# Optimization experiments

Hardware: AMD Instinct MI355X
Metric: run time of the kernel (lower is better)

Reference implementation:

```python
import jax, jax.numpy as jnp
import numpy as np

DIM = 8          # per-head dim
ATT_EPS = 1e-15
BN_EPS = 1e-6


def setup_inputs() -> dict:
    key = jax.random.key(0)
    ks = jax.random.split(key, 6)
    B, C, H, W = 8, 256, 64, 64
    td = 256                      # heads * dim = 32 * 8
    return {
        'x':      jax.random.normal(ks[0], (B, C, H, W), jnp.float32),
        'w_qkv':  jax.random.normal(ks[1], (3 * td, C), jnp.float32) * 0.05,
        'w_dw':   jax.random.normal(ks[2], (3 * td, 1, 5, 5), jnp.float32) * 0.05,
        'w_pw':   jax.random.normal(ks[3], (96, 8, 8), jnp.float32) * 0.05,   # (groups, out/g, in/g)
        'w_proj': jax.random.normal(ks[4], (C, 2 * td), jnp.float32) * 0.05,
        'bn_gamma': jnp.ones((C,), jnp.float32),
        'bn_beta':  jnp.zeros((C,), jnp.float32),
        'bn_mean':  jnp.zeros((C,), jnp.float32),
        'bn_var':   jnp.ones((C,), jnp.float32),
    }


def _relu_linear_att(ms, H, W):
    # ms: [B, C, H, W] with C = heads * 3*DIM
    B = ms.shape[0]
    d = DIM
    qkv = ms.reshape(B, -1, 3 * d, H * W).transpose(0, 1, 3, 2)   # [B, h, N, 3d]
    q = jax.nn.relu(qkv[..., :d])
    k = jax.nn.relu(qkv[..., d:2 * d])
    v = qkv[..., 2 * d:]
    v = jnp.pad(v, ((0, 0), (0, 0), (0, 0), (0, 1)), constant_values=1.0)  # ones column
    kv = jnp.einsum('bhnd,bhne->bhde', k, v)                       # [B, h, d, d+1]
    out = jnp.einsum('bhnd,bhde->bhne', q, kv)                     # [B, h, N, d+1]
    out = out[..., :-1] / (out[..., -1:] + ATT_EPS)
    return out.transpose(0, 1, 3, 2).reshape(B, -1, H, W)          # [B, h*d, H, W]


def reference(x, w_qkv, w_dw, w_pw, w_proj, bn_gamma, bn_beta, bn_mean, bn_var):
    B, C, H, W = x.shape
    # 1x1 qkv projection
    qkv = jnp.einsum('oc,bchw->bohw', w_qkv, x)                    # [B, 768, H, W]
    # multiscale aggregation: 5x5 depthwise then grouped 1x1 (groups = 3*heads = 96)
    dw = jax.lax.conv_general_dilated(
        qkv, w_dw, window_strides=(1, 1), padding=[(2, 2), (2, 2)],
        dimension_numbers=('NCHW', 'OIHW', 'NCHW'),
        feature_group_count=qkv.shape[1])
    G, O, I = w_pw.shape
    agg = jnp.einsum('goi,bgihw->bgohw', w_pw,
                     dw.reshape(B, G, I, H, W)).reshape(B, G * O, H, W)
    ms = jnp.concatenate([qkv, agg], axis=1)                       # [B, 1536, H, W]
    att = _relu_linear_att(ms, H, W)                               # [B, 512, H, W]
    # proj: 1x1 conv + BatchNorm (eval mode) + identity activation
    p = jnp.einsum('oc,bchw->bohw', w_proj, att)                   # [B, 256, H, W]
    inv = bn_gamma / jnp.sqrt(bn_var + BN_EPS)
    p = p * inv[None, :, None, None] + (bn_beta - bn_mean * inv)[None, :, None, None]
    return x + p
```

## Files before the change

### kernel.cpp

```cpp
#include <hip/hip_runtime.h>
#include <hip/hip_bf16.h>


#define HW 4096
#define ATT_EPS 1e-15f
#define BN_EPS 1e-6f

typedef __attribute__((ext_vector_type(8))) short short8;
typedef __attribute__((ext_vector_type(4))) short short4v;
typedef __attribute__((ext_vector_type(4))) float f32x4;
typedef __attribute__((ext_vector_type(2))) float f32x2;
typedef __attribute__((ext_vector_type(8))) unsigned short u16x8;
typedef __attribute__((ext_vector_type(4))) unsigned short u16x4;

static __device__ inline short f2bf(float f) {
    union { float f; unsigned u; } v; v.f = f;
    unsigned r = v.u + 0x7fff + ((v.u >> 16) & 1);
    return (short)(r >> 16);
}
static __device__ inline float bf2f(unsigned short u) {
    union { unsigned u; float f; } v; v.u = (unsigned)u << 16; return v.f;
}

__global__ __launch_bounds__(256) void prep_w(const float* __restrict__ wproj,
                                              unsigned short* __restrict__ wbf) {
    const int i = (blockIdx.x * 256 + threadIdx.x) * 4;
    float4 v = *(const float4*)&wproj[i];
    u16x4 r = {(unsigned short)f2bf(v.x), (unsigned short)f2bf(v.y),
               (unsigned short)f2bf(v.z), (unsigned short)f2bf(v.w)};
    *(u16x4*)&wbf[i] = r;
}

__global__ __launch_bounds__(256) void qkv_gemm(const float* __restrict__ x,
                                                const float* __restrict__ w,
                                                unsigned short* __restrict__ qkv) {
    __shared__ short A_l[128 * 40];
    __shared__ short B_l[128 * 40];
    const int t  = threadIdx.x;
    const int b  = blockIdx.z;
    const int ob = blockIdx.y * 128;
    const int nb = blockIdx.x * 128;
    const float* xb = x + (size_t)b * 256 * HW;

    const int lane = t & 63, wave = t >> 6;
    const int wo = (wave >> 1) * 64, wn = (wave & 1) * 64;

    f32x4 acc[4][4];
#pragma unroll
    for (int s = 0; s < 4; s++)
#pragma unroll
        for (int u = 0; u < 4; u++) acc[s][u] = (f32x4){0.f, 0.f, 0.f, 0.f};

    const int col4 = (t & 7) * 4;
    const int r0   = t >> 3;
    for (int kb = 0; kb < 256; kb += 32) {
        __syncthreads();
#pragma unroll
        for (int i = 0; i < 4; i++) {
            const int r = r0 + 32 * i;
            float4 v = *(const float4*)&w[(ob + r) * 256 + kb + col4];
            short4v s4 = {f2bf(v.x), f2bf(v.y), f2bf(v.z), f2bf(v.w)};
            *(short4v*)&A_l[r * 40 + col4] = s4;
        }
#pragma unroll
        for (int i = 0; i < 4; i++) {
            const int n4 = (t & 7) + 8 * i;
            float4 v = *(const float4*)&xb[(size_t)(kb + r0) * HW + nb + n4 * 4];
            B_l[(n4 * 4 + 0) * 40 + r0] = f2bf(v.x);
            B_l[(n4 * 4 + 1) * 40 + r0] = f2bf(v.y);
            B_l[(n4 * 4 + 2) * 40 + r0] = f2bf(v.z);
            B_l[(n4 * 4 + 3) * 40 + r0] = f2bf(v.w);
        }
        __syncthreads();

        short8 af[4], bf[4];
#pragma unroll
        for (int s = 0; s < 4; s++)
            af[s] = *(const short8*)&A_l[(wo + s * 16 + (lane & 15)) * 40 + (lane >> 4) * 8];
#pragma unroll
        for (int u = 0; u < 4; u++)
            bf[u] = *(const short8*)&B_l[(wn + u * 16 + (lane & 15)) * 40 + (lane >> 4) * 8];
#pragma unroll
        for (int s = 0; s < 4; s++)
#pragma unroll
            for (int u = 0; u < 4; u++)
                acc[s][u] = __builtin_amdgcn_mfma_f32_16x16x32_bf16(af[s], bf[u], acc[s][u], 0, 0, 0);
    }

#pragma unroll
    for (int s = 0; s < 4; s++)
#pragma unroll
        for (int u = 0; u < 4; u++)
#pragma unroll
            for (int r = 0; r < 4; r++) {
                const int o = ob + wo + s * 16 + (lane >> 4) * 4 + r;
                const int n = nb + wn + u * 16 + (lane & 15);
                qkv[((size_t)b * 768 + o) * HW + n] = (unsigned short)f2bf(acc[s][u][r]);
            }
}

__global__ __launch_bounds__(256, 6) void dw_agg(const unsigned short* __restrict__ qkv,
                                                 const float* __restrict__ wdw,
                                                 const float* __restrict__ wpw,
                                                 unsigned short* __restrict__ agg) {
    __shared__ float tile_raw[8 + 4 * 20 * 64 + 8];
    float* tile = tile_raw + 8;
    const int b = blockIdx.z, g = blockIdx.y;
    const int y0 = blockIdx.x * 16;
    const int t = threadIdx.x;
    const int tx = t & 15, ty = t >> 4;

    const float* wkg = wdw + g * 8 * 25;
    const float* pwg = wpw + g * 64;

    float out[8][4];
#pragma unroll
    for (int o = 0; o < 8; o++)
#pragma unroll
        for (int j = 0; j < 4; j++) out[o][j] = 0.f;

#pragma unroll 1
    for (int half = 0; half < 2; half++) {
        if (half) __syncthreads();
#pragma unroll
        for (int k = 0; k < 3; k++) {
            const int i = t + 256 * k;
            if (i < 640) {
                const int c8 = i & 7, rr = (i >> 3) % 20, ch = i / 160;
                const int y = y0 - 2 + rr;
                u16x8 v = {0, 0, 0, 0, 0, 0, 0, 0};
                if (y >= 0 && y < 64)
                    v = *(const u16x8*)&qkv[((size_t)(b * 768 + g * 8 + half * 4 + ch)) * HW + y * 64 + c8 * 8];
                f32x4 lo = {bf2f(v[0]), bf2f(v[1]), bf2f(v[2]), bf2f(v[3])};
                f32x4 hi = {bf2f(v[4]), bf2f(v[5]), bf2f(v[6]), bf2f(v[7])};
                *(f32x4*)&tile[i * 8]     = lo;
                *(f32x4*)&tile[i * 8 + 4] = hi;
            }
        }
        __syncthreads();

#pragma unroll 1
        for (int ch4 = 0; ch4 < 4; ch4++) {
            const int ch = half * 4 + ch4;
            const float* wkc = wkg + ch * 25;
            float a0 = 0.f, a1 = 0.f, a2 = 0.f, a3 = 0.f;
#pragma unroll
            for (int dy = 0; dy < 5; dy++) {
                const int off = ch4 * 1280 + (ty + dy) * 64 + tx * 4;
                f32x4 C = *(const f32x4*)&tile[off];
                f32x2 L = *(const f32x2*)&tile[off - 2];
                f32x2 R = *(const f32x2*)&tile[off + 4];
                float win[8];
                win[0] = (tx == 0)  ? 0.f : L[0];
                win[1] = (tx == 0)  ? 0.f : L[1];
                win[2] = C[0]; win[3] = C[1];
                win[4] = C[2]; win[5] = C[3];
                win[6] = (tx == 15) ? 0.f : R[0];
                win[7] = (tx == 15) ? 0.f : R[1];
#pragma unroll
                for (int dx = 0; dx < 5; dx++) {
                    const float wv = wkc[dy * 5 + dx];
                    a0 += wv * win[dx + 0];
                    a1 += wv * win[dx + 1];
                    a2 += wv * win[dx + 2];
                    a3 += wv * win[dx + 3];
                }
            }
#pragma unroll
            for (int o = 0; o < 8; o++) {
                const float wv = pwg[o * 8 + ch];
                out[o][0] += wv * a0; out[o][1] += wv * a1;
                out[o][2] += wv * a2; out[o][3] += wv * a3;
            }
        }
    }

#pragma unroll
    for (int o = 0; o < 8; o++) {
        u16x4 rv = {(unsigned short)f2bf(out[o][0]), (unsigned short)f2bf(out[o][1]),
                    (unsigned short)f2bf(out[o][2]), (unsigned short)f2bf(out[o][3])};
        *(u16x4*)&agg[((size_t)(b * 768 + g * 8 + o)) * HW + (y0 + ty) * 64 + tx * 4] = rv;
    }
}

__global__ __launch_bounds__(256) void kv_pass(const unsigned short* __restrict__ qkv,
                                               const unsigned short* __restrict__ agg,
                                               float* __restrict__ kvpart) {
    const int h = blockIdx.x, b = blockIdx.y, c = blockIdx.z;
    const unsigned short* buf = (h < 32) ? qkv : agg;
    const int cbase = (h & 31) * 24;
    const u16x4* kp4 = (const u16x4*)(buf + ((size_t)b * 768 + cbase + 8)  * HW);
    const u16x4* vp4 = (const u16x4*)(buf + ((size_t)b * 768 + cbase + 16) * HW);

    const int nn = c * 256 + threadIdx.x;

    float kk[8][4];
#pragma unroll
    for (int d = 0; d < 8; d++) {
        u16x4 v = kp4[d * 1024 + nn];
        kk[d][0] = fmaxf(bf2f(v.x), 0.f); kk[d][1] = fmaxf(bf2f(v.y), 0.f);
        kk[d][2] = fmaxf(bf2f(v.z), 0.f); kk[d][3] = fmaxf(bf2f(v.w), 0.f);
    }

    float acc[8][9];
#pragma unroll
    for (int e = 0; e < 8; e++) {
        u16x4 vr = vp4[e * 1024 + nn];
        float v0 = bf2f(vr.x), v1 = bf2f(vr.y), v2 = bf2f(vr.z), v3 = bf2f(vr.w);
#pragma unroll
        for (int d = 0; d < 8; d++)
            acc[d][e] = kk[d][0] * v0 + kk[d][1] * v1 + kk[d][2] * v2 + kk[d][3] * v3;
    }
#pragma unroll
    for (int d = 0; d < 8; d++)
        acc[d][8] = kk[d][0] + kk[d][1] + kk[d][2] + kk[d][3];

    __shared__ float red[4][72];
    const int lane = threadIdx.x & 63, wv = threadIdx.x >> 6;
#pragma unroll
    for (int d = 0; d < 8; d++) {
#pragma unroll
        for (int e = 0; e < 9; e++) {
            float v = acc[d][e];
            v += __shfl_xor(v, 1);  v += __shfl_xor(v, 2);
            v += __shfl_xor(v, 4);  v += __shfl_xor(v, 8);
            v += __shfl_xor(v, 16); v += __shfl_xor(v, 32);
            if (lane == 0) red[wv][d * 9 + e] = v;
        }
    }
    __syncthreads();
    if (threadIdx.x < 72) {
        float s = red[0][threadIdx.x] + red[1][threadIdx.x] +
                  red[2][threadIdx.x] + red[3][threadIdx.x];
        kvpart[(size_t)c * 36864 + ((size_t)(b * 64 + h)) * 72 + threadIdx.x] = s;
    }
}

__global__ __launch_bounds__(256) void kv_red(const float* __restrict__ kvpart,
                                              float* __restrict__ kvout) {
    const int i = blockIdx.x * 256 + threadIdx.x;
    kvout[i] = (kvpart[i] + kvpart[36864 + i]) +
               (kvpart[2 * 36864 + i] + kvpart[3 * 36864 + i]);
}

__global__ __launch_bounds__(256) void att_pass(const unsigned short* __restrict__ qkv,
                                                const unsigned short* __restrict__ agg,
                                                const float* __restrict__ kvbuf,
                                                unsigned short* __restrict__ att_f) {
    const int h = blockIdx.y, b = blockIdx.z;
    const int t = threadIdx.x;
    const float* kvp = kvbuf + ((size_t)(b * 64 + h)) * 72;

    float kvr[72];
#pragma unroll
    for (int i = 0; i < 18; i++) {
        f32x4 v = *(const f32x4*)&kvp[i * 4];
        kvr[i * 4 + 0] = v[0]; kvr[i * 4 + 1] = v[1];
        kvr[i * 4 + 2] = v[2]; kvr[i * 4 + 3] = v[3];
    }

    const unsigned short* buf = (h < 32) ? qkv : agg;
    const int cbase = (h & 31) * 24;
    const int n0 = (blockIdx.x * 256 + t) * 8;
    const unsigned short* qp = buf + ((size_t)b * 768 + cbase) * HW + n0;

    float q[8][8];
#pragma unroll
    for (int d = 0; d < 8; d++) {
        u16x8 v = *(const u16x8*)&qp[(size_t)d * HW];
#pragma unroll
        for (int j = 0; j < 8; j++) q[d][j] = fmaxf(bf2f(v[j]), 0.f);
    }

    unsigned short* op = att_f + (((size_t)(b * 64 + h)) * HW + n0) * 8;
#pragma unroll
    for (int j = 0; j < 8; j++) {
        float num[9];
#pragma unroll
        for (int e = 0; e < 9; e++) num[e] = 0.f;
#pragma unroll
        for (int d = 0; d < 8; d++) {
            const float qv = q[d][j];
#pragma unroll
            for (int e = 0; e < 9; e++) num[e] += qv * kvr[d * 9 + e];
        }
        const float rden = 1.f / (num[8] + ATT_EPS);
        u16x8 r;
#pragma unroll
        for (int e = 0; e < 8; e++) r[e] = (unsigned short)f2bf(num[e] * rden);
        *(u16x8*)&op[j * 8] = r;
    }
}

__global__ __launch_bounds__(256) void proj_gemm(const unsigned short* __restrict__ wbf,
                                                 const unsigned short* __restrict__ att_f,
                                                 const float* __restrict__ gamma,
                                                 const float* __restrict__ beta,
                                                 const float* __restrict__ mean,
                                                 const float* __restrict__ var,
                                                 const float* __restrict__ x,
                                                 float* __restrict__ out) {
    const int t  = threadIdx.x;
    const int b  = blockIdx.z;
    const int ob = blockIdx.y * 128;
    const int nb = blockIdx.x * 128;
    const int lane = t & 63, wave = t >> 6;
    const int wo = (wave >> 1) * 64, wn = (wave & 1) * 64;

    const int am = lane & 15, ak = lane >> 4;
    const unsigned short* ap0 = wbf + (size_t)(ob + wo + am) * 512 + ak * 8;
    const unsigned short* bp0 = att_f +
        (((size_t)b * 64 + ak) * HW + nb + wn + am) * 8;

    f32x4 acc[4][4];
#pragma unroll
    for (int s = 0; s < 4; s++)
#pragma unroll
        for (int u = 0; u < 4; u++) acc[s][u] = (f32x4){0.f, 0.f, 0.f, 0.f};

    for (int kb = 0; kb < 512; kb += 32) {
        short8 af[4], bf[4];
#pragma unroll
        for (int s = 0; s < 4; s++)
            af[s] = *(const short8*)(ap0 + (size_t)s * 16 * 512 + kb);
#pragma unroll
        for (int u = 0; u < 4; u++)
            bf[u] = *(const short8*)(bp0 + ((size_t)(kb >> 3) * HW + u * 16) * 8);
#pragma unroll
        for (int s = 0; s < 4; s++)
#pragma unroll
            for (int u = 0; u < 4; u++)
                acc[s][u] = __builtin_amdgcn_mfma_f32_16x16x32_bf16(af[s], bf[u], acc[s][u], 0, 0, 0);
    }

#pragma unroll
    for (int s = 0; s < 4; s++) {
        const int o_base = ob + wo + s * 16 + (lane >> 4) * 4;
#pragma unroll
        for (int r = 0; r < 4; r++) {
            const int o = o_base + r;
            const float inv = gamma[o] * rsqrtf(var[o] + BN_EPS);
            const float sh  = beta[o] - mean[o] * inv;
#pragma unroll
            for (int u = 0; u < 4; u++) {
                const int n = nb + wn + u * 16 + (lane & 15);
                const size_t idx = ((size_t)b * 256 + o) * HW + n;
                out[idx] = x[idx] + acc[s][u][r] * inv + sh;
            }
        }
    }
}

extern "C" void kernel_launch(void* const* d_in, const int* in_sizes, int n_in,
                              void* d_out, int out_size, void* d_ws, size_t ws_size,
                              hipStream_t stream) {
    const float* x      = (const float*)d_in[0];
    const float* w_qkv  = (const float*)d_in[1];
    const float* w_dw   = (const float*)d_in[2];
    const float* w_pw   = (const float*)d_in[3];
    const float* w_proj = (const float*)d_in[4];
    const float* gamma  = (const float*)d_in[5];
    const float* beta   = (const float*)d_in[6];
    const float* mean   = (const float*)d_in[7];
    const float* var    = (const float*)d_in[8];
    float* out = (float*)d_out;

    unsigned short* qkv  = (unsigned short*)d_ws;
    unsigned short* agg  = qkv + (size_t)25165824;
    unsigned short* attf = agg + (size_t)25165824;
    unsigned short* wbf  = attf + (size_t)16777216;
    float* kvb = (float*)(wbf + (size_t)131072);
    float* kvpart = (float*)attf;

    prep_w  <<<dim3(128),       256, 0, stream>>>(w_proj, wbf);
    qkv_gemm<<<dim3(32, 6, 8),  256, 0, stream>>>(x, w_qkv, qkv);
    dw_agg  <<<dim3(4, 96, 8),  256, 0, stream>>>(qkv, w_dw, w_pw, agg);
    kv_pass <<<dim3(64, 8, 4),  256, 0, stream>>>(qkv, agg, kvpart);
    kv_red  <<<dim3(144),       256, 0, stream>>>(kvpart, kvb);
    att_pass<<<dim3(2, 64, 8),  256, 0, stream>>>(qkv, agg, kvb, attf);
    proj_gemm<<<dim3(32, 2, 8), 256, 0, stream>>>(wbf, attf,
                                                  gamma, beta, mean, var, x, out);
}
```

Baseline: 249.9 us.

## Compute KV outer products with bf16 MFMA per wave over head pairs

Rewrites the kv_pass kernel so each wave computes K^T[V|1] for two heads using 16x16x32 bf16 MFMA instructions, with ReLU applied via sign-bit masking and a constant ones row standing in for the normalizer column. This replaces per-thread FMA accumulation and the long shuffle plus shared-memory reductions. The sequence is now split into 16 chunks instead of 4, so kv_red sums 16 partials. The partial buffer grows fourfold and reuses the att buffer region; the kv stage is a small share of total time.

```diff
diff --git a/kernel.cpp b/kernel.cpp
--- a/kernel.cpp
+++ b/kernel.cpp
@@ -186,61 +186,66 @@
 __global__ __launch_bounds__(256) void kv_pass(const unsigned short* __restrict__ qkv,
                                                const unsigned short* __restrict__ agg,
                                                float* __restrict__ kvpart) {
-    const int h = blockIdx.x, b = blockIdx.y, c = blockIdx.z;
-    const unsigned short* buf = (h < 32) ? qkv : agg;
-    const int cbase = (h & 31) * 24;
-    const u16x4* kp4 = (const u16x4*)(buf + ((size_t)b * 768 + cbase + 8)  * HW);
-    const u16x4* vp4 = (const u16x4*)(buf + ((size_t)b * 768 + cbase + 16) * HW);
-
-    const int nn = c * 256 + threadIdx.x;
-
-    float kk[8][4];
-#pragma unroll
-    for (int d = 0; d < 8; d++) {
-        u16x4 v = kp4[d * 1024 + nn];
-        kk[d][0] = fmaxf(bf2f(v.x), 0.f); kk[d][1] = fmaxf(bf2f(v.y), 0.f);
-        kk[d][2] = fmaxf(bf2f(v.z), 0.f); kk[d][3] = fmaxf(bf2f(v.w), 0.f);
-    }
-
-    float acc[8][9];
-#pragma unroll
-    for (int e = 0; e < 8; e++) {
-        u16x4 vr = vp4[e * 1024 + nn];
-        float v0 = bf2f(vr.x), v1 = bf2f(vr.y), v2 = bf2f(vr.z), v3 = bf2f(vr.w);
-#pragma unroll
-        for (int d = 0; d < 8; d++)
-            acc[d][e] = kk[d][0] * v0 + kk[d][1] * v1 + kk[d][2] * v2 + kk[d][3] * v3;
-    }
-#pragma unroll
-    for (int d = 0; d < 8; d++)
-        acc[d][8] = kk[d][0] + kk[d][1] + kk[d][2] + kk[d][3];
-
-    __shared__ float red[4][72];
-    const int lane = threadIdx.x & 63, wv = threadIdx.x >> 6;
-#pragma unroll
-    for (int d = 0; d < 8; d++) {
-#pragma unroll
-        for (int e = 0; e < 9; e++) {
-            float v = acc[d][e];
-            v += __shfl_xor(v, 1);  v += __shfl_xor(v, 2);
-            v += __shfl_xor(v, 4);  v += __shfl_xor(v, 8);
-            v += __shfl_xor(v, 16); v += __shfl_xor(v, 32);
-            if (lane == 0) red[wv][d * 9 + e] = v;
-        }
-    }
-    __syncthreads();
-    if (threadIdx.x < 72) {
-        float s = red[0][threadIdx.x] + red[1][threadIdx.x] +
-                  red[2][threadIdx.x] + red[3][threadIdx.x];
-        kvpart[(size_t)c * 36864 + ((size_t)(b * 64 + h)) * 72 + threadIdx.x] = s;
+    const int t = threadIdx.x;
+    const int w = t >> 6, lane = t & 63;
+    const int hp = blockIdx.x * 4 + w;
+    const int b = blockIdx.y, c = blockIdx.z;
+    const int h0 = hp * 2, h1 = h0 + 1;
+    const unsigned short* buf = (h0 < 32) ? qkv : agg;
+    const int cb0 = (h0 & 31) * 24, cb1 = (h1 & 31) * 24;
+
+    const int row = lane & 15, kgrp = lane >> 4;
+    const int n0 = c * 256 + kgrp * 8;
+
+    const int chA = (row < 8) ? (cb0 + 8 + row) : (cb1 + row);
+    const unsigned short* ap = buf + ((size_t)b * 768 + chA) * HW + n0;
+
+    const bool bload = (row < 8);
+    const unsigned short* bp0 = buf + ((size_t)b * 768 + cb0 + 16 + (row & 7)) * HW + n0;
+    const unsigned short* bp1 = buf + ((size_t)b * 768 + cb1 + 16 + (row & 7)) * HW + n0;
+    const short cfill = (row == 8) ? (short)0x3F80 : (short)0;
+    const short8 bconst = {cfill, cfill, cfill, cfill, cfill, cfill, cfill, cfill};
+
+    f32x4 acc0 = {0.f, 0.f, 0.f, 0.f};
+    f32x4 acc1 = {0.f, 0.f, 0.f, 0.f};
+
+#pragma unroll
+    for (int i = 0; i < 8; i++) {
+        u16x8 av = *(const u16x8*)(ap + i * 32);
+        short8 b0 = bload ? *(const short8*)(bp0 + i * 32) : bconst;
+        short8 b1 = bload ? *(const short8*)(bp1 + i * 32) : bconst;
+        short8 ar;
+#pragma unroll
+        for (int j = 0; j < 8; j++)
+            ar[j] = (short)((av[j] & 0x8000) ? 0 : av[j]);
+        acc0 = __builtin_amdgcn_mfma_f32_16x16x32_bf16(ar, b0, acc0, 0, 0, 0);
+        acc1 = __builtin_amdgcn_mfma_f32_16x16x32_bf16(ar, b1, acc1, 0, 0, 0);
+    }
+
+    if (row <= 8) {
+        float* kp;
+        f32x4 a;
+        int dbase;
+        if (kgrp < 2) {
+            kp = kvpart + (size_t)c * 36864 + (size_t)(b * 64 + h0) * 72;
+            a = acc0; dbase = kgrp * 4;
+        } else {
+            kp = kvpart + (size_t)c * 36864 + (size_t)(b * 64 + h1) * 72;
+            a = acc1; dbase = (kgrp - 2) * 4;
+        }
+#pragma unroll
+        for (int r = 0; r < 4; r++)
+            kp[(dbase + r) * 9 + row] = a[r];
     }
 }
 
 __global__ __launch_bounds__(256) void kv_red(const float* __restrict__ kvpart,
                                               float* __restrict__ kvout) {
     const int i = blockIdx.x * 256 + threadIdx.x;
-    kvout[i] = (kvpart[i] + kvpart[36864 + i]) +
-               (kvpart[2 * 36864 + i] + kvpart[3 * 36864 + i]);
+    float s = 0.f;
+#pragma unroll
+    for (int c = 0; c < 16; c++) s += kvpart[(size_t)c * 36864 + i];
+    kvout[i] = s;
 }
 
 __global__ __launch_bounds__(256) void att_pass(const unsigned short* __restrict__ qkv,
@@ -375,7 +380,7 @@
     prep_w  <<<dim3(128),       256, 0, stream>>>(w_proj, wbf);
     qkv_gemm<<<dim3(32, 6, 8),  256, 0, stream>>>(x, w_qkv, qkv);
     dw_agg  <<<dim3(4, 96, 8),  256, 0, stream>>>(qkv, w_dw, w_pw, agg);
-    kv_pass <<<dim3(64, 8, 4),  256, 0, stream>>>(qkv, agg, kvpart);
+    kv_pass <<<dim3(8, 8, 16),  256, 0, stream>>>(qkv, agg, kvpart);
     kv_red  <<<dim3(144),       256, 0, stream>>>(kvpart, kvb);
     att_pass<<<dim3(2, 64, 8),  256, 0, stream>>>(qkv, agg, kvb, attf);
     proj_gemm<<<dim3(32, 2, 8), 256, 0, stream>>>(wbf, attf,
```

Measured after the change: 220.8 us. 1.13x faster.
